# Optimization experiments

Measured on AMD Instinct MI355X. Metric: run time of the kernel, lower is better.

Reference implementation:

```python
import jax, jax.numpy as jnp
import numpy as np

EPS = 1e-3  # keras LayerNormalization default epsilon


def _layernorm(x, gamma, beta):
    mu = jnp.mean(x, axis=-1, keepdims=True)
    var = jnp.mean(jnp.square(x - mu), axis=-1, keepdims=True)
    return (x - mu) * jax.lax.rsqrt(var + EPS) * gamma + beta


def setup_inputs() -> dict:
    key = jax.random.key(0)
    B, T, D, H = 8, 2048, 192, 3
    KD = D           # TalkingHeadsAttention(key_dim=dim, value_dim=dim)
    HID = 4 * D      # mlp_ratio = 4.0
    ks = jax.random.split(key, 12)
    s_in = 0.02
    inp = {
        "x": jax.random.normal(ks[0], (B, T, D), jnp.float32),
        # norm1 / norm2
        "gamma1": jnp.ones((D,), jnp.float32),
        "beta1": jnp.zeros((D,), jnp.float32),
        "gamma2": jnp.ones((D,), jnp.float32),
        "beta2": jnp.zeros((D,), jnp.float32),
        # attention projections (qkv_bias=False -> no biases)
        "wq": jax.random.normal(ks[1], (D, H, KD), jnp.float32) * s_in,
        "wk": jax.random.normal(ks[2], (D, H, KD), jnp.float32) * s_in,
        "wv": jax.random.normal(ks[3], (D, H, KD), jnp.float32) * s_in,
        "wo": jax.random.normal(ks[4], (H, KD, D), jnp.float32) * s_in,
        # talking-heads mixing matrices [H, H]
        "pre_w": jnp.eye(H, dtype=jnp.float32) + jax.random.normal(ks[5], (H, H), jnp.float32) * 0.02,
        "post_w": jnp.eye(H, dtype=jnp.float32) + jax.random.normal(ks[6], (H, H), jnp.float32) * 0.02,
        # MLP (bias=True)
        "w1": jax.random.normal(ks[7], (D, HID), jnp.float32) * s_in,
        "b1": jnp.zeros((HID,), jnp.float32),
        "w2": jax.random.normal(ks[8], (HID, D), jnp.float32) * s_in,
        "b2": jnp.zeros((D,), jnp.float32),
    }
    return inp


def reference(x, gamma1, beta1, gamma2, beta2, wq, wk, wv, wo, pre_w, post_w, w1, b1, w2, b2):
    KD = wq.shape[-1]
    # --- pre-norm + talking-heads attention ---
    n = _layernorm(x, gamma1, beta1)                      # [B,T,D]
    q = jnp.einsum("btd,dhk->bthk", n, wq)               # [B,T,H,KD]
    k = jnp.einsum("bsd,dhk->bshk", n, wk)
    v = jnp.einsum("bsd,dhk->bshk", n, wv)
    scores = jnp.einsum("bthk,bshk->bhts", q, k) / jnp.sqrt(jnp.asarray(KD, x.dtype))
    scores = jnp.einsum("bhts,hg->bgts", scores, pre_w)   # pre-softmax head mix
    probs = jax.nn.softmax(scores, axis=-1)
    probs = jnp.einsum("bhts,hg->bgts", probs, post_w)    # post-softmax head mix
    ctx = jnp.einsum("bhts,bshk->bthk", probs, v)         # [B,T,H,KD]
    attn_out = jnp.einsum("bthk,hkd->btd", ctx, wo)       # [B,T,D]
    x = x + attn_out                                      # ls1/drop_path1 are Identity
    # --- pre-norm + MLP ---
    n2 = _layernorm(x, gamma2, beta2)
    h = jax.nn.gelu(n2 @ w1 + b1, approximate=False)      # keras gelu = exact erf
    mlp_out = h @ w2 + b2
    return x + mlp_out
```

## Files before the change

### kernel.cpp

```cpp
#include <hip/hip_runtime.h>
#include <hip/hip_bf16.h>

typedef __hip_bfloat16 bf16;
typedef unsigned char u8;
typedef __attribute__((ext_vector_type(8))) __bf16 bf16x8;
typedef __attribute__((ext_vector_type(4))) float f32x4;

__device__ __forceinline__ void gld_lds16(const void* g, void* l) {
  __builtin_amdgcn_global_load_lds((const __attribute__((address_space(1))) void*)g,
                                   (__attribute__((address_space(3))) void*)l, 16, 0, 0);
}
__device__ __forceinline__ u8 f2e4m3(float v) {
  return (u8)(__builtin_amdgcn_cvt_pk_fp8_f32(v, 0.f, 0, false) & 0xff);
}

__global__ __launch_bounds__(256) void prep_weights(
    const float* __restrict__ wq, const float* __restrict__ wk,
    const float* __restrict__ w1, const float* __restrict__ w2,
    bf16* __restrict__ WqkvT, bf16* __restrict__ w1T, bf16* __restrict__ w2T)
{
  int i = blockIdx.x * 256 + threadIdx.x;
  if (i < 221184) {
    int n = i / 192, d = i % 192;
    int sel = n / 576, c = n % 576, h = c / 192, kd = c % 192;
    const float* w = (sel == 0) ? wq : wk;
    WqkvT[i] = __float2bfloat16(w[(d*3 + h)*192 + kd]);
    return;
  }
  i -= 221184;
  if (i < 147456) {
    int j = i / 192, d = i % 192;
    w1T[i] = __float2bfloat16(w1[d*768 + j]);
    return;
  }
  i -= 147456;
  if (i < 147456) {
    int d = i / 768, j = i % 768;
    w2T[i] = __float2bfloat16(w2[j*192 + d]);
  }
}

__global__ __launch_bounds__(192) void wm_k(
    const float* __restrict__ wv, const float* __restrict__ wo,
    const float* __restrict__ post_w, bf16* __restrict__ WqkvT)
{
  const int dd = threadIdx.x;
  const int h  = blockIdx.x / 192;
  const int din = blockIdx.x % 192;
  float acc = 0.f;
  #pragma unroll
  for (int g2 = 0; g2 < 3; ++g2) {
    const float pw = post_w[h*3 + g2];
    const float* wvp = wv + (size_t)din*576 + g2*192;
    const float* wop = wo + (size_t)(g2*192)*192 + dd;
    float s = 0.f;
    for (int kd = 0; kd < 192; ++kd)
      s += wvp[kd] * wop[(size_t)kd*192];
    acc += pw * s;
  }
  WqkvT[(size_t)(1152 + h*192 + dd)*192 + din] = __float2bfloat16(acc);
}

__global__ __launch_bounds__(256) void ln_k(const float* __restrict__ x,
    const float* __restrict__ gamma, const float* __restrict__ beta,
    bf16* __restrict__ out)
{
  int row = blockIdx.x * 4 + (threadIdx.x >> 6);
  int lane = threadIdx.x & 63;
  const float* xr = x + (size_t)row * 192;
  float v0 = xr[lane], v1 = xr[lane + 64], v2 = xr[lane + 128];
  float s = v0 + v1 + v2;
  #pragma unroll
  for (int o = 32; o; o >>= 1) s += __shfl_xor(s, o);
  float mu = s * (1.f / 192.f);
  float d0 = v0 - mu, d1 = v1 - mu, d2 = v2 - mu;
  float q = d0*d0 + d1*d1 + d2*d2;
  #pragma unroll
  for (int o = 32; o; o >>= 1) q += __shfl_xor(q, o);
  float rs = rsqrtf(q * (1.f / 192.f) + 1e-3f);
  bf16* orow = out + (size_t)row * 192;
  orow[lane]       = __float2bfloat16(d0*rs*gamma[lane]       + beta[lane]);
  orow[lane + 64]  = __float2bfloat16(d1*rs*gamma[lane + 64]  + beta[lane + 64]);
  orow[lane + 128] = __float2bfloat16(d2*rs*gamma[lane + 128] + beta[lane + 128]);
}

enum { EPI_QKV = 0, EPI_GELU = 3, EPI_OUT = 4 };

template<int EPI>
__global__ __launch_bounds__(256) void gemm_bt(
    const bf16* __restrict__ A, const bf16* __restrict__ BT,
    int M, int N, int K,
    float* __restrict__ outF, bf16* __restrict__ outB,
    const float* __restrict__ bias,
    u8* __restrict__ q_out, u8* __restrict__ k_out, u8* __restrict__ mt_out)
{
  const int tid = threadIdx.x, lane = tid & 63, wid = tid >> 6;
  const int wm = wid >> 1, wn = wid & 1;
  const int row0 = blockIdx.y * 128, col0 = blockIdx.x * 64;
  __shared__ __align__(16) bf16 As[2][128 * 32];
  __shared__ __align__(16) bf16 Bs[2][64 * 32];
  f32x4 acc[4][2] = {};
  const int NT = K >> 5;

#define STAGE(buf_, kt_) do { \
    const bf16* Ab_ = A + (size_t)row0 * K + (kt_) * 32; \
    int c0_ = tid, r0_ = c0_ >> 2, cc0_ = (c0_ & 3) << 3; \
    gld_lds16(Ab_ + (size_t)r0_ * K + cc0_, &As[buf_][c0_ * 8]); \
    int c1_ = tid + 256, r1_ = c1_ >> 2, cc1_ = (c1_ & 3) << 3; \
    gld_lds16(Ab_ + (size_t)r1_ * K + cc1_, &As[buf_][c1_ * 8]); \
    const bf16* Bb_ = BT + (size_t)col0 * K + (kt_) * 32; \
    gld_lds16(Bb_ + (size_t)(tid >> 2) * K + ((tid & 3) << 3), &Bs[buf_][tid * 8]); \
  } while (0)

  STAGE(0, 0);
  for (int kt = 0; kt < NT; ++kt) {
    __syncthreads();
    const int buf = kt & 1;
    if (kt + 1 < NT) STAGE(buf ^ 1, kt + 1);
    const int koff = (lane >> 4) * 8;
    bf16x8 af[4], bfr[2];
    #pragma unroll
    for (int m = 0; m < 4; ++m)
      af[m] = *(const bf16x8*)&As[buf][(wm*64 + m*16 + (lane & 15))*32 + koff];
    #pragma unroll
    for (int n = 0; n < 2; ++n)
      bfr[n] = *(const bf16x8*)&Bs[buf][(wn*32 + n*16 + (lane & 15))*32 + koff];
    #pragma unroll
    for (int m = 0; m < 4; ++m)
      #pragma unroll
      for (int n = 0; n < 2; ++n)
        acc[m][n] = __builtin_amdgcn_mfma_f32_16x16x32_bf16(af[m], bfr[n], acc[m][n], 0, 0, 0);
  }
#undef STAGE

  const int rbase = row0 + wm * 64;
  const int cbase = col0 + wn * 32;
  #pragma unroll
  for (int m = 0; m < 4; ++m) {
    #pragma unroll
    for (int n = 0; n < 2; ++n) {
      const int col = cbase + n*16 + (lane & 15);
      const int rtop = rbase + m*16 + ((lane >> 4) << 2);
      if constexpr (EPI == EPI_QKV) {
        const int b = rtop >> 11, t_ = rtop & 2047;
        const int sel = col / 576, c2 = col % 576;
        const int h = c2 / 192, kd = c2 % 192;
        if (sel == 2) {
          int pk = __builtin_amdgcn_cvt_pk_fp8_f32(acc[m][n][0], acc[m][n][1], 0, false);
          pk = __builtin_amdgcn_cvt_pk_fp8_f32(acc[m][n][2], acc[m][n][3], pk, true);
          const size_t fo = ((((size_t)b*64 + (t_>>5))*3 + h)*12 + (kd>>4))*512
                          + (((kd&15) + (((t_>>3)&3)<<4))<<3) + (t_&4);
          *(unsigned*)&mt_out[fo] = (unsigned)pk;
        } else {
          #pragma unroll
          for (int j = 0; j < 4; ++j) {
            const int t = t_ + j;
            const size_t fo = ((((size_t)b*64 + (t>>5))*3 + h)*6 + (kd>>5))*1024
                            + (((t>>4)&1))*512
                            + (((t&15) + (((kd>>3)&3)<<4))<<3) + (kd&7);
            if (sel == 0) q_out[fo] = f2e4m3(acc[m][n][j]);
            else          k_out[fo] = f2e4m3(acc[m][n][j]);
          }
        }
      } else {
        #pragma unroll
        for (int j = 0; j < 4; ++j) {
          const int row = rtop + j;
          const float v = acc[m][n][j];
          if constexpr (EPI == EPI_GELU) {
            const float u = v + bias[col];
            outB[(size_t)row * 768 + col] =
                __float2bfloat16(0.5f * u * (1.f + erff(u * 0.70710678118654752f)));
          } else if constexpr (EPI == EPI_OUT) {
            const size_t idx = (size_t)row * 192 + col;
            outF[idx] = outF[idx] + v + bias[col];
          }
        }
      }
    }
  }
}

__global__ __launch_bounds__(256, 2) void attn_k(
    const u8* __restrict__ q, const u8* __restrict__ kf,
    const u8* __restrict__ MT, const float* __restrict__ pre_w,
    const float* __restrict__ x, float* __restrict__ out)
{
  const int tid = threadIdx.x, lane = tid & 63, wv = tid >> 6;
  const int l15 = lane & 15, l4 = lane >> 4;
  const int tq = wv & 1, sq = wv >> 1;
  const int bid = blockIdx.x;
  const int b = bid & 7;
  const int tt = bid >> 3;
  const int t0 = tt * 32;

  __shared__ __align__(16) u8 Ks[2][18432];
  __shared__ __align__(16) u8 Ps[2][3072];
  __shared__ float rlPart[2][3][32];

  const u8* qfb = q + ((size_t)b*64 + tt) * 18432;
  long qf[3][6];
  #pragma unroll
  for (int h = 0; h < 3; ++h)
    #pragma unroll
    for (int kq = 0; kq < 6; ++kq)
      qf[h][kq] = *(const long*)(qfb + ((h*6 + kq)*2 + tq)*512 + lane*8);

  float pwf[9];
  #pragma unroll
  for (int i = 0; i < 9; ++i) pwf[i] = pre_w[i] * 0.07216878364870323f * 1.44269504088896f;

  f32x4 acc[3][2][3] = {};
  float sgacc[3] = {0.f, 0.f, 0.f};
  const int trow = tq*16 + l15;
  const int psw = (l15 >> 2) & 3;
  const int pwr = (((sq*2 + (l4 >> 1)) ^ psw) << 3) + ((l4 & 1) << 2);
  const int prd = (l4 ^ psw) << 3;

  const u8* kfb = kf + (size_t)b * 64 * 18432;
  const u8* mtb = MT + (size_t)b * 64 * 18432;

#define STAGEK(buf_, st_) do { \
    const u8* kb_ = kfb + (size_t)(st_) * 18432; \
    _Pragma("unroll") \
    for (int i_ = 0; i_ < 5; ++i_) { \
      const int L_ = i_ * 256 + tid; \
      if (L_ < 1152) gld_lds16(kb_ + L_*16, &Ks[buf_][L_*16]); \
    } \
  } while (0)

#define LOADMF(MF_, st_) do { \
    const u8* mb_ = mtb + (size_t)(st_) * 18432 + wv*3*512 + lane*8; \
    _Pragma("unroll") \
    for (int g_ = 0; g_ < 3; ++g_) \
      _Pragma("unroll") \
      for (int n_ = 0; n_ < 3; ++n_) \
        MF_[g_][n_] = *(const long*)(mb_ + (g_*12 + n_)*512); \
  } while (0)

#define PV(stm1_, MF_) do { \
    const int bp_ = (stm1_) & 1; \
    __builtin_amdgcn_s_setprio(1); \
    _Pragma("unroll") \
    for (int g_ = 0; g_ < 3; ++g_) \
      _Pragma("unroll") \
      for (int m_ = 0; m_ < 2; ++m_) { \
        const long pf_ = *(const long*)&Ps[bp_][g_*1024 + (m_*16 + l15)*32 + prd]; \
        _Pragma("unroll") \
        for (int n_ = 0; n_ < 3; ++n_) \
          acc[g_][m_][n_] = __builtin_amdgcn_mfma_f32_16x16x32_fp8_fp8(pf_, MF_[g_][n_], acc[g_][m_][n_], 0, 0, 0); \
      } \
    __builtin_amdgcn_s_setprio(0); \
  } while (0)

#define QKSM(st_) do { \
    const int bq_ = (st_) & 1; \
    f32x4 sacc0 = {}, sacc1 = {}, sacc2 = {}; \
    __builtin_amdgcn_s_setprio(1); \
    _Pragma("unroll") \
    for (int kq_ = 0; kq_ < 6; ++kq_) { \
      const long kf0_ = *(const long*)&Ks[bq_][((0*6 + kq_)*2 + sq)*512 + lane*8]; \
      sacc0 = __builtin_amdgcn_mfma_f32_16x16x32_fp8_fp8(kf0_, qf[0][kq_], sacc0, 0, 0, 0); \
      const long kf1_ = *(const long*)&Ks[bq_][((1*6 + kq_)*2 + sq)*512 + lane*8]; \
      sacc1 = __builtin_amdgcn_mfma_f32_16x16x32_fp8_fp8(kf1_, qf[1][kq_], sacc1, 0, 0, 0); \
      const long kf2_ = *(const long*)&Ks[bq_][((2*6 + kq_)*2 + sq)*512 + lane*8]; \
      sacc2 = __builtin_amdgcn_mfma_f32_16x16x32_fp8_fp8(kf2_, qf[2][kq_], sacc2, 0, 0, 0); \
    } \
    __builtin_amdgcn_s_setprio(0); \
    _Pragma("unroll") \
    for (int g_ = 0; g_ < 3; ++g_) { \
      float e0_ = exp2f(sacc0[0]*pwf[g_] + sacc1[0]*pwf[3+g_] + sacc2[0]*pwf[6+g_]); \
      float e1_ = exp2f(sacc0[1]*pwf[g_] + sacc1[1]*pwf[3+g_] + sacc2[1]*pwf[6+g_]); \
      float e2_ = exp2f(sacc0[2]*pwf[g_] + sacc1[2]*pwf[3+g_] + sacc2[2]*pwf[6+g_]); \
      float e3_ = exp2f(sacc0[3]*pwf[g_] + sacc1[3]*pwf[3+g_] + sacc2[3]*pwf[6+g_]); \
      sgacc[g_] += (e0_ + e1_) + (e2_ + e3_); \
      int pk_ = __builtin_amdgcn_cvt_pk_fp8_f32(e0_, e1_, 0, false); \
      pk_ = __builtin_amdgcn_cvt_pk_fp8_f32(e2_, e3_, pk_, true); \
      *(unsigned*)&Ps[bq_][g_*1024 + trow*32 + pwr] = (unsigned)pk_; \
    } \
  } while (0)

  long mfA[3][3], mfB[3][3];

  STAGEK(0, 0);
  __syncthreads();
  STAGEK(1, 1);
  LOADMF(mfA, 0);
  QKSM(0);
  for (int st = 1; st < 63; st += 2) {
    __syncthreads();
    STAGEK((st + 1) & 1, st + 1);
    LOADMF(mfB, st);
    PV(st - 1, mfA);
    QKSM(st);
    __syncthreads();
    if (st + 2 < 64) STAGEK((st + 2) & 1, st + 2);
    LOADMF(mfA, st + 1);
    PV(st, mfB);
    QKSM(st + 1);
  }
  __syncthreads();
  LOADMF(mfB, 63);
  PV(62, mfA);
  QKSM(63);
  __syncthreads();
  PV(63, mfB);
  #pragma unroll
  for (int g = 0; g < 3; ++g) {
    float s = sgacc[g];
    s += __shfl_xor(s, 16);
    s += __shfl_xor(s, 32);
    if (l4 == 0) rlPart[sq][g][trow] = s;
  }
  __syncthreads();

  #pragma unroll
  for (int m = 0; m < 2; ++m) {
    #pragma unroll
    for (int j = 0; j < 4; ++j) {
      const int row = m*16 + l4*4 + j;
      float rlv[3];
      #pragma unroll
      for (int g = 0; g < 3; ++g)
        rlv[g] = 1.f / (rlPart[0][g][row] + rlPart[1][g][row]);
      #pragma unroll
      for (int n = 0; n < 3; ++n) {
        const int d = wv*48 + n*16 + l15;
        const size_t idx = ((size_t)b*2048 + t0 + row)*192 + d;
        out[idx] = x[idx] + rlv[0]*acc[0][m][n][j] + rlv[1]*acc[1][m][n][j]
                          + rlv[2]*acc[2][m][n][j];
      }
    }
  }
#undef STAGEK
#undef LOADMF
#undef PV
#undef QKSM
}

extern "C" void kernel_launch(void* const* d_in, const int* in_sizes, int n_in,
                              void* d_out, int out_size, void* d_ws, size_t ws_size,
                              hipStream_t stream)
{
  (void)in_sizes; (void)n_in; (void)out_size; (void)ws_size;
  const float* x      = (const float*)d_in[0];
  const float* gamma1 = (const float*)d_in[1];
  const float* beta1  = (const float*)d_in[2];
  const float* gamma2 = (const float*)d_in[3];
  const float* beta2  = (const float*)d_in[4];
  const float* wq     = (const float*)d_in[5];
  const float* wk     = (const float*)d_in[6];
  const float* wv     = (const float*)d_in[7];
  const float* wo     = (const float*)d_in[8];
  const float* pre_w  = (const float*)d_in[9];
  const float* post_w = (const float*)d_in[10];
  const float* w1     = (const float*)d_in[11];
  const float* b1     = (const float*)d_in[12];
  const float* w2     = (const float*)d_in[13];
  const float* b2     = (const float*)d_in[14];
  float* out = (float*)d_out;

  uint8_t* base = (uint8_t*)d_ws;
  size_t off = 0;
  auto alloc = [&](size_t bytes) {
    uint8_t* r = base + off; off += (bytes + 255) & ~(size_t)255; return r;
  };
  bf16* nb      = (bf16*)alloc((size_t)16384 * 192 * 2);
  u8*   qb      = (u8*)alloc((size_t)9437184);
  u8*   kb      = (u8*)alloc((size_t)9437184);
  u8*   MTslab  = (u8*)alloc((size_t)9437184);
  bf16* WqkvT   = (bf16*)alloc((size_t)331776 * 2);
  bf16* w1T     = (bf16*)alloc((size_t)147456 * 2);
  bf16* w2T     = (bf16*)alloc((size_t)147456 * 2);
  bf16* hb      = (bf16*)qb;

  prep_weights<<<2016, 256, 0, stream>>>(wq, wk, w1, w2, WqkvT, w1T, w2T);
  wm_k<<<576, 192, 0, stream>>>(wv, wo, post_w, WqkvT);
  ln_k<<<4096, 256, 0, stream>>>(x, gamma1, beta1, nb);
  gemm_bt<EPI_QKV><<<dim3(27, 128, 1), 256, 0, stream>>>(nb, WqkvT, 16384, 1728, 192,
      nullptr, nullptr, nullptr, qb, kb, MTslab);
  attn_k<<<512, 256, 0, stream>>>(qb, kb, MTslab, pre_w, x, out);
  ln_k<<<4096, 256, 0, stream>>>(out, gamma2, beta2, nb);
  gemm_bt<EPI_GELU><<<dim3(12, 128, 1), 256, 0, stream>>>(nb, w1T, 16384, 768, 192,
      nullptr, hb, b1, nullptr, nullptr, nullptr);
  gemm_bt<EPI_OUT><<<dim3(3, 128, 1), 256, 0, stream>>>(hb, w2T, 16384, 192, 768,
      out, nullptr, b2, nullptr, nullptr, nullptr);
}
```

Baseline: 197.6 us.

## Fuse second LayerNorm into attention epilogue, pack softmax FMAs, shrink out-GEMM tile

The attention kernel's epilogue now computes per-row sum and sum of squares across its four waves through shared memory and writes the normalized bf16 activations directly. This removes the separate ln_k launch and its re-read of the residual. The pre-softmax head-mix math uses packed v_pk_mul/v_pk_fma on pairs of scores to halve VALU instruction count. The final GEMM uses a 64-row tile so it launches more blocks (768 instead of 384) for better occupancy. The variance now uses E[x^2]-mu^2, which is slightly less numerically robust.

```diff
diff --git a/kernel.cpp b/kernel.cpp
--- a/kernel.cpp
+++ b/kernel.cpp
@@ -5,6 +5,7 @@
 typedef unsigned char u8;
 typedef __attribute__((ext_vector_type(8))) __bf16 bf16x8;
 typedef __attribute__((ext_vector_type(4))) float f32x4;
+typedef __attribute__((ext_vector_type(2))) float f32x2;
 
 __device__ __forceinline__ void gld_lds16(const void* g, void* l) {
   __builtin_amdgcn_global_load_lds((const __attribute__((address_space(1))) void*)g,
@@ -12,6 +13,16 @@
 }
 __device__ __forceinline__ u8 f2e4m3(float v) {
   return (u8)(__builtin_amdgcn_cvt_pk_fp8_f32(v, 0.f, 0, false) & 0xff);
+}
+__device__ __forceinline__ f32x2 pk_mul(f32x2 a, f32x2 b) {
+  f32x2 d;
+  asm("v_pk_mul_f32 %0, %1, %2" : "=v"(d) : "v"(a), "v"(b));
+  return d;
+}
+__device__ __forceinline__ f32x2 pk_fma(f32x2 a, f32x2 b, f32x2 c) {
+  f32x2 d;
+  asm("v_pk_fma_f32 %0, %1, %2, %3" : "=v"(d) : "v"(a), "v"(b), "v"(c));
+  return d;
 }
 
 __global__ __launch_bounds__(256) void prep_weights(
@@ -86,7 +97,7 @@
 
 enum { EPI_QKV = 0, EPI_GELU = 3, EPI_OUT = 4 };
 
-template<int EPI>
+template<int EPI, int MROWS = 128>
 __global__ __launch_bounds__(256) void gemm_bt(
     const bf16* __restrict__ A, const bf16* __restrict__ BT,
     int M, int N, int K,
@@ -94,20 +105,23 @@
     const float* __restrict__ bias,
     u8* __restrict__ q_out, u8* __restrict__ k_out, u8* __restrict__ mt_out)
 {
+  constexpr int MB = MROWS / 32;
   const int tid = threadIdx.x, lane = tid & 63, wid = tid >> 6;
   const int wm = wid >> 1, wn = wid & 1;
-  const int row0 = blockIdx.y * 128, col0 = blockIdx.x * 64;
-  __shared__ __align__(16) bf16 As[2][128 * 32];
+  const int row0 = blockIdx.y * MROWS, col0 = blockIdx.x * 64;
+  __shared__ __align__(16) bf16 As[2][MROWS * 32];
   __shared__ __align__(16) bf16 Bs[2][64 * 32];
-  f32x4 acc[4][2] = {};
+  f32x4 acc[MB][2] = {};
   const int NT = K >> 5;
 
 #define STAGE(buf_, kt_) do { \
     const bf16* Ab_ = A + (size_t)row0 * K + (kt_) * 32; \
     int c0_ = tid, r0_ = c0_ >> 2, cc0_ = (c0_ & 3) << 3; \
     gld_lds16(Ab_ + (size_t)r0_ * K + cc0_, &As[buf_][c0_ * 8]); \
-    int c1_ = tid + 256, r1_ = c1_ >> 2, cc1_ = (c1_ & 3) << 3; \
-    gld_lds16(Ab_ + (size_t)r1_ * K + cc1_, &As[buf_][c1_ * 8]); \
+    if constexpr (MROWS == 128) { \
+      int c1_ = tid + 256, r1_ = c1_ >> 2, cc1_ = (c1_ & 3) << 3; \
+      gld_lds16(Ab_ + (size_t)r1_ * K + cc1_, &As[buf_][c1_ * 8]); \
+    } \
     const bf16* Bb_ = BT + (size_t)col0 * K + (kt_) * 32; \
     gld_lds16(Bb_ + (size_t)(tid >> 2) * K + ((tid & 3) << 3), &Bs[buf_][tid * 8]); \
   } while (0)
@@ -118,25 +132,25 @@
     const int buf = kt & 1;
     if (kt + 1 < NT) STAGE(buf ^ 1, kt + 1);
     const int koff = (lane >> 4) * 8;
-    bf16x8 af[4], bfr[2];
-    #pragma unroll
-    for (int m = 0; m < 4; ++m)
-      af[m] = *(const bf16x8*)&As[buf][(wm*64 + m*16 + (lane & 15))*32 + koff];
+    bf16x8 af[MB], bfr[2];
+    #pragma unroll
+    for (int m = 0; m < MB; ++m)
+      af[m] = *(const bf16x8*)&As[buf][(wm*(MROWS/2) + m*16 + (lane & 15))*32 + koff];
     #pragma unroll
     for (int n = 0; n < 2; ++n)
       bfr[n] = *(const bf16x8*)&Bs[buf][(wn*32 + n*16 + (lane & 15))*32 + koff];
     #pragma unroll
-    for (int m = 0; m < 4; ++m)
+    for (int m = 0; m < MB; ++m)
       #pragma unroll
       for (int n = 0; n < 2; ++n)
         acc[m][n] = __builtin_amdgcn_mfma_f32_16x16x32_bf16(af[m], bfr[n], acc[m][n], 0, 0, 0);
   }
 #undef STAGE
 
-  const int rbase = row0 + wm * 64;
+  const int rbase = row0 + wm * (MROWS/2);
   const int cbase = col0 + wn * 32;
   #pragma unroll
-  for (int m = 0; m < 4; ++m) {
+  for (int m = 0; m < MB; ++m) {
     #pragma unroll
     for (int n = 0; n < 2; ++n) {
       const int col = cbase + n*16 + (lane & 15);
@@ -184,7 +198,9 @@
 __global__ __launch_bounds__(256, 2) void attn_k(
     const u8* __restrict__ q, const u8* __restrict__ kf,
     const u8* __restrict__ MT, const float* __restrict__ pre_w,
-    const float* __restrict__ x, float* __restrict__ out)
+    const float* __restrict__ x, const float* __restrict__ gamma2,
+    const float* __restrict__ beta2, float* __restrict__ out,
+    bf16* __restrict__ nb)
 {
   const int tid = threadIdx.x, lane = tid & 63, wv = tid >> 6;
   const int l15 = lane & 15, l4 = lane >> 4;
@@ -197,6 +213,7 @@
   __shared__ __align__(16) u8 Ks[2][18432];
   __shared__ __align__(16) u8 Ps[2][3072];
   __shared__ float rlPart[2][3][32];
+  __shared__ float lnS[4][32][2];
 
   const u8* qfb = q + ((size_t)b*64 + tt) * 18432;
   long qf[3][6];
@@ -206,9 +223,12 @@
     for (int kq = 0; kq < 6; ++kq)
       qf[h][kq] = *(const long*)(qfb + ((h*6 + kq)*2 + tq)*512 + lane*8);
 
-  float pwf[9];
-  #pragma unroll
-  for (int i = 0; i < 9; ++i) pwf[i] = pre_w[i] * 0.07216878364870323f * 1.44269504088896f;
+  f32x2 pwf2[9];
+  #pragma unroll
+  for (int i = 0; i < 9; ++i) {
+    const float v = pre_w[i] * 0.07216878364870323f * 1.44269504088896f;
+    pwf2[i][0] = v; pwf2[i][1] = v;
+  }
 
   f32x4 acc[3][2][3] = {};
   float sgacc[3] = {0.f, 0.f, 0.f};
@@ -267,12 +287,19 @@
       sacc2 = __builtin_amdgcn_mfma_f32_16x16x32_fp8_fp8(kf2_, qf[2][kq_], sacc2, 0, 0, 0); \
     } \
     __builtin_amdgcn_s_setprio(0); \
+    f32x2 p0a = {sacc0[0], sacc0[1]}, p0b = {sacc0[2], sacc0[3]}; \
+    f32x2 p1a = {sacc1[0], sacc1[1]}, p1b = {sacc1[2], sacc1[3]}; \
+    f32x2 p2a = {sacc2[0], sacc2[1]}, p2b = {sacc2[2], sacc2[3]}; \
     _Pragma("unroll") \
     for (int g_ = 0; g_ < 3; ++g_) { \
-      float e0_ = exp2f(sacc0[0]*pwf[g_] + sacc1[0]*pwf[3+g_] + sacc2[0]*pwf[6+g_]); \
-      float e1_ = exp2f(sacc0[1]*pwf[g_] + sacc1[1]*pwf[3+g_] + sacc2[1]*pwf[6+g_]); \
-      float e2_ = exp2f(sacc0[2]*pwf[g_] + sacc1[2]*pwf[3+g_] + sacc2[2]*pwf[6+g_]); \
-      float e3_ = exp2f(sacc0[3]*pwf[g_] + sacc1[3]*pwf[3+g_] + sacc2[3]*pwf[6+g_]); \
+      f32x2 va = pk_mul(p0a, pwf2[g_]); \
+      va = pk_fma(p1a, pwf2[3+g_], va); \
+      va = pk_fma(p2a, pwf2[6+g_], va); \
+      f32x2 vb = pk_mul(p0b, pwf2[g_]); \
+      vb = pk_fma(p1b, pwf2[3+g_], vb); \
+      vb = pk_fma(p2b, pwf2[6+g_], vb); \
+      float e0_ = exp2f(va[0]), e1_ = exp2f(va[1]); \
+      float e2_ = exp2f(vb[0]), e3_ = exp2f(vb[1]); \
       sgacc[g_] += (e0_ + e1_) + (e2_ + e3_); \
       int pk_ = __builtin_amdgcn_cvt_pk_fp8_f32(e0_, e1_, 0, false); \
       pk_ = __builtin_amdgcn_cvt_pk_fp8_f32(e2_, e3_, pk_, true); \
@@ -314,6 +341,7 @@
   }
   __syncthreads();
 
+  float ovv[2][3][4];
   #pragma unroll
   for (int m = 0; m < 2; ++m) {
     #pragma unroll
@@ -323,12 +351,44 @@
       #pragma unroll
       for (int g = 0; g < 3; ++g)
         rlv[g] = 1.f / (rlPart[0][g][row] + rlPart[1][g][row]);
+      float s = 0.f, ss = 0.f;
       #pragma unroll
       for (int n = 0; n < 3; ++n) {
         const int d = wv*48 + n*16 + l15;
         const size_t idx = ((size_t)b*2048 + t0 + row)*192 + d;
-        out[idx] = x[idx] + rlv[0]*acc[0][m][n][j] + rlv[1]*acc[1][m][n][j]
-                          + rlv[2]*acc[2][m][n][j];
+        const float ov = x[idx] + rlv[0]*acc[0][m][n][j] + rlv[1]*acc[1][m][n][j]
+                                + rlv[2]*acc[2][m][n][j];
+        out[idx] = ov;
+        ovv[m][n][j] = ov;
+        s += ov; ss += ov*ov;
+      }
+      #pragma unroll
+      for (int o = 1; o < 16; o <<= 1) { s += __shfl_xor(s, o); ss += __shfl_xor(ss, o); }
+      if (l15 == 0) { lnS[wv][row][0] = s; lnS[wv][row][1] = ss; }
+    }
+  }
+  __syncthreads();
+
+  float gmL[3], btL[3];
+  #pragma unroll
+  for (int n = 0; n < 3; ++n) {
+    const int d = wv*48 + n*16 + l15;
+    gmL[n] = gamma2[d]; btL[n] = beta2[d];
+  }
+  #pragma unroll
+  for (int m = 0; m < 2; ++m) {
+    #pragma unroll
+    for (int j = 0; j < 4; ++j) {
+      const int row = m*16 + l4*4 + j;
+      const float ts  = lnS[0][row][0] + lnS[1][row][0] + lnS[2][row][0] + lnS[3][row][0];
+      const float tss = lnS[0][row][1] + lnS[1][row][1] + lnS[2][row][1] + lnS[3][row][1];
+      const float mu = ts * (1.f / 192.f);
+      const float rs = rsqrtf(tss * (1.f / 192.f) - mu*mu + 1e-3f);
+      #pragma unroll
+      for (int n = 0; n < 3; ++n) {
+        const int d = wv*48 + n*16 + l15;
+        nb[((size_t)b*2048 + t0 + row)*192 + d] =
+            __float2bfloat16((ovv[m][n][j] - mu) * rs * gmL[n] + btL[n]);
       }
     }
   }
@@ -377,12 +437,11 @@
   prep_weights<<<2016, 256, 0, stream>>>(wq, wk, w1, w2, WqkvT, w1T, w2T);
   wm_k<<<576, 192, 0, stream>>>(wv, wo, post_w, WqkvT);
   ln_k<<<4096, 256, 0, stream>>>(x, gamma1, beta1, nb);
-  gemm_bt<EPI_QKV><<<dim3(27, 128, 1), 256, 0, stream>>>(nb, WqkvT, 16384, 1728, 192,
+  gemm_bt<EPI_QKV, 128><<<dim3(27, 128, 1), 256, 0, stream>>>(nb, WqkvT, 16384, 1728, 192,
       nullptr, nullptr, nullptr, qb, kb, MTslab);
-  attn_k<<<512, 256, 0, stream>>>(qb, kb, MTslab, pre_w, x, out);
-  ln_k<<<4096, 256, 0, stream>>>(out, gamma2, beta2, nb);
-  gemm_bt<EPI_GELU><<<dim3(12, 128, 1), 256, 0, stream>>>(nb, w1T, 16384, 768, 192,
+  attn_k<<<512, 256, 0, stream>>>(qb, kb, MTslab, pre_w, x, gamma2, beta2, out, nb);
+  gemm_bt<EPI_GELU, 128><<<dim3(12, 128, 1), 256, 0, stream>>>(nb, w1T, 16384, 768, 192,
       nullptr, hb, b1, nullptr, nullptr, nullptr);
-  gemm_bt<EPI_OUT><<<dim3(3, 128, 1), 256, 0, stream>>>(hb, w2T, 16384, 192, 768,
+  gemm_bt<EPI_OUT, 64><<<dim3(3, 256, 1), 256, 0, stream>>>(hb, w2T, 16384, 192, 768,
       out, nullptr, b2, nullptr, nullptr, nullptr);
 }
```

New measurement: 195.8 us. No clear change (-0.9%).
